# Optimization experiments

Measured on AMD Instinct MI355X. Metric: run time of the kernel, lower is better.

Reference implementation:

```python
import jax, jax.numpy as jnp
import numpy as np

GX, GY, GZ = 128, 128, 16   # voxel_range
N = 100000                  # occupied voxels
C = 64                      # channels (inc == outc)
K = 27                      # 3x3x3 kernel offsets
EPS = 1e-5
NEG_SLOPE = 0.01            # LeakyReLU default


def _kernel_map():
    """Build sparse-conv neighbor map: nbr[k, n] = row index of the input voxel at
    coord[n] + offset[k], or N (sentinel -> zero feature) if unoccupied/out of range."""
    rng = np.random.RandomState(0)
    flat = rng.choice(GX * GY * GZ, size=N, replace=False)
    x = flat // (GY * GZ)
    rem = flat % (GY * GZ)
    y = rem // GZ
    z = rem % GZ
    lut = np.full(GX * GY * GZ, N, dtype=np.int32)
    lut[flat] = np.arange(N, dtype=np.int32)
    offs = [(i, j, k) for i in (-1, 0, 1) for j in (-1, 0, 1) for k in (-1, 0, 1)]
    nbr = np.full((K, N), N, dtype=np.int32)
    for ki, (dx, dy, dz) in enumerate(offs):
        xs, ys, zs = x + dx, y + dy, z + dz
        valid = (xs >= 0) & (xs < GX) & (ys >= 0) & (ys < GY) & (zs >= 0) & (zs < GZ)
        fl = (np.clip(xs, 0, GX - 1) * (GY * GZ)
              + np.clip(ys, 0, GY - 1) * GZ
              + np.clip(zs, 0, GZ - 1))
        nbr[ki] = np.where(valid, lut[fl], N)
    return jnp.asarray(nbr)


def setup_inputs() -> dict:
    key = jax.random.key(0)
    k0, k1, k2 = jax.random.split(key, 3)
    w_scale = 1.0 / np.sqrt(C * K)  # Minkowski-style fan-in init
    return {
        "feats": jax.random.normal(k0, (N, C), jnp.float32),
        "W1": jax.random.normal(k1, (K, C, C), jnp.float32) * w_scale,
        "g1": jnp.ones((C,), jnp.float32),
        "b1": jnp.zeros((C,), jnp.float32),
        "W2": jax.random.normal(k2, (K, C, C), jnp.float32) * w_scale,
        "g2": jnp.ones((C,), jnp.float32),
        "b2": jnp.zeros((C,), jnp.float32),
        "nbr_idx": _kernel_map(),
    }


def _sparse_conv(f, W, nbr):
    # gather-GEMM-scatter: fp has a zero sentinel row at index N
    fp = jnp.concatenate([f, jnp.zeros((1, f.shape[1]), f.dtype)], axis=0)
    g = fp[nbr]                                # [K, N, Cin] gathered neighbors
    return jnp.einsum('knc,kco->no', g, W)     # [N, Cout]


def _bn(x, gamma, beta):
    # training-mode BatchNorm over all active voxels, per channel
    m = jnp.mean(x, axis=0)
    v = jnp.var(x, axis=0)
    return (x - m) * jax.lax.rsqrt(v + EPS) * gamma + beta


def _lrelu(x):
    return jnp.where(x >= 0, x, NEG_SLOPE * x)


def reference(feats, W1, g1, b1, W2, g2, b2, nbr_idx):
    skip = feats  # downsample is identity (inc == outc, stride == 1)
    y = _lrelu(_bn(_sparse_conv(feats, W1, nbr_idx), g1, b1))
    y = _lrelu(_bn(_sparse_conv(y, W2, nbr_idx), g2, b2))
    return _lrelu(skip + y)
```

## Files before the change

kernel.cpp:

```cpp
#include <hip/hip_runtime.h>
#include <hip/hip_bf16.h>


#define N_VOX 100000
#define NCH 64
#define NK 27
#define ROWS 128
#define NBLK ((N_VOX + ROWS - 1) / ROWS)

typedef __hip_bfloat16 bf16;
typedef __attribute__((ext_vector_type(8))) short bf16x8;
typedef __attribute__((ext_vector_type(4))) float f32x4;

__device__ __forceinline__ float b2f(short s) {
  unsigned u = ((unsigned)(unsigned short)s) << 16;
  return __builtin_bit_cast(float, u);
}
__device__ __forceinline__ short f2b(float f) {
  __hip_bfloat16 h = __float2bfloat16(f);
  return __builtin_bit_cast(short, h);
}

__device__ __forceinline__ void gload16(const void* g, void* l) {
  __builtin_amdgcn_global_load_lds(
      (const __attribute__((address_space(1))) void*)g,
      (__attribute__((address_space(3))) void*)l, 16, 0, 0);
}

__global__ void cast_feats(const float* __restrict__ feats, bf16* __restrict__ fbf) {
  const size_t i = ((size_t)blockIdx.x * 256 + threadIdx.x) * 8;
  if (i >= (size_t)(N_VOX + 1) * NCH) return;
  bf16x8 o;
  if (i < (size_t)N_VOX * NCH) {
    const f32x4 v0 = *reinterpret_cast<const f32x4*>(feats + i);
    const f32x4 v1 = *reinterpret_cast<const f32x4*>(feats + i + 4);
#pragma unroll
    for (int e = 0; e < 8; ++e) o[e] = f2b(e < 4 ? v0[e] : v1[e - 4]);
  } else {
#pragma unroll
    for (int e = 0; e < 8; ++e) o[e] = 0;
  }
  *reinterpret_cast<bf16x8*>((short*)fbf + i) = o;
}

__global__ void pack_w(const float* __restrict__ W1, const float* __restrict__ W2,
                       bf16* __restrict__ wp1, bf16* __restrict__ wp2) {
  const int t = blockIdx.x * 256 + threadIdx.x;
  const int half = NK * 4 * 2 * 64;
  if (t >= 2 * half) return;
  const float* W = (t < half) ? W1 : W2;
  short* wp = (short*)((t < half) ? wp1 : wp2);
  const int q = (t < half) ? t : t - half;
  const int l  = q & 63;
  const int kb = (q >> 6) & 1;
  const int j  = (q >> 7) & 3;
  const int k  = q >> 9;
  const int oo = j * 16 + (l & 15);
  const int c0 = kb * 32 + (l >> 4) * 8;
  bf16x8 v;
#pragma unroll
  for (int e = 0; e < 8; ++e)
    v[e] = f2b(W[((size_t)k * 64 + c0 + e) * 64 + oo]);
  *reinterpret_cast<bf16x8*>(&wp[(size_t)q * 8]) = v;
}

__global__ __launch_bounds__(256, 2)
void conv_mfma(const bf16* __restrict__ feat, const bf16* __restrict__ wp,
               const int* __restrict__ nbr, bf16* __restrict__ y,
               float* __restrict__ part) {
  __shared__ short GA[2][ROWS * NCH];
  __shared__ short GB[2][8 * 512];
  __shared__ int nbrL[NK * ROWS];
  __shared__ float redS[4][NCH];
  __shared__ float redQ[4][NCH];

  const int tid = threadIdx.x;
  const int lane = tid & 63;
  const int wv = tid >> 6;

  const int nwg = NBLK;
  const int xcd = blockIdx.x & 7;
  const int pos = blockIdx.x >> 3;
  const int q8 = nwg >> 3, r8 = nwg & 7;
  const int bid = (xcd < r8 ? xcd * (q8 + 1) : r8 * (q8 + 1) + (xcd - r8) * q8) + pos;
  const int n0 = bid * ROWS;

  for (int t = tid; t < NK * ROWS; t += 256) {
    const int k = t >> 7;
    const int rr = t & (ROWS - 1);
    nbrL[t] = (n0 + rr < N_VOX) ? nbr[(size_t)k * N_VOX + n0 + rr] : N_VOX;
  }
  __syncthreads();

  f32x4 acc[2][4];
#pragma unroll
  for (int h = 0; h < 2; ++h)
#pragma unroll
    for (int j = 0; j < 4; ++j)
      acc[h][j] = (f32x4){0.f, 0.f, 0.f, 0.f};

  auto stage = [&](int buf, int k) {
#pragma unroll
    for (int i = 0; i < 4; ++i) {
      const int s = i * 256 + wv * 64 + lane;
      const int row = s >> 3;
      const int p = (s & 7) ^ (row & 7);
      const int idx = nbrL[k * ROWS + row];
      const bf16* src = feat + (size_t)idx * NCH + p * 8;
      gload16((const void*)src, (void*)&GA[buf][(i * 256 + wv * 64) * 8]);
    }
#pragma unroll
    for (int t = 0; t < 2; ++t) {
      const int f = wv * 2 + t;
      const short* src = (const short*)wp + ((size_t)k * 8 + f) * 512 + lane * 8;
      gload16((const void*)src, (void*)&GB[buf][f * 512]);
    }
  };

  stage(0, 0);
  stage(1, 1);

  for (int k = 0; k < NK; ++k) {
    if (k < NK - 1) asm volatile("s_waitcnt vmcnt(6)" ::: "memory");
    else            asm volatile("s_waitcnt vmcnt(0)" ::: "memory");
    __builtin_amdgcn_sched_barrier(0);
    __builtin_amdgcn_s_barrier();

    const int cur = k & 1;

    bf16x8 Bf[4][2];
#pragma unroll
    for (int j = 0; j < 4; ++j)
#pragma unroll
      for (int kb = 0; kb < 2; ++kb)
        Bf[j][kb] = *reinterpret_cast<const bf16x8*>(
            &GB[cur][(j * 2 + kb) * 512 + lane * 8]);

    bf16x8 Af[2][2];
#pragma unroll
    for (int h = 0; h < 2; ++h)
#pragma unroll
      for (int kb = 0; kb < 2; ++kb) {
        const int rr = wv * 32 + h * 16 + (lane & 15);
        const int p = (kb * 4 + (lane >> 4)) ^ (rr & 7);
        Af[h][kb] = *reinterpret_cast<const bf16x8*>(&GA[cur][rr * NCH + p * 8]);
      }

#pragma unroll
    for (int h = 0; h < 2; ++h)
#pragma unroll
      for (int j = 0; j < 4; ++j)
#pragma unroll
        for (int kb = 0; kb < 2; ++kb)
          acc[h][j] = __builtin_amdgcn_mfma_f32_16x16x32_bf16(
              Af[h][kb], Bf[j][kb], acc[h][j], 0, 0, 0);

    __builtin_amdgcn_s_barrier();
    __builtin_amdgcn_sched_barrier(0);
    if (k + 2 < NK) stage(cur, k + 2);
  }

#pragma unroll
  for (int h = 0; h < 2; ++h)
#pragma unroll
    for (int j = 0; j < 4; ++j) {
      const int col = j * 16 + (lane & 15);
#pragma unroll
      for (int r = 0; r < 4; ++r) {
        const int row = n0 + wv * 32 + h * 16 + (lane >> 4) * 4 + r;
        if (row < N_VOX) ((short*)y)[(size_t)row * NCH + col] = f2b(acc[h][j][r]);
      }
    }

#pragma unroll
  for (int j = 0; j < 4; ++j) {
    float s1 = 0.f, s2 = 0.f;
#pragma unroll
    for (int h = 0; h < 2; ++h)
#pragma unroll
      for (int r = 0; r < 4; ++r) {
        const float v = acc[h][j][r];
        s1 += v;
        s2 += v * v;
      }
    s1 += __shfl_xor(s1, 16); s2 += __shfl_xor(s2, 16);
    s1 += __shfl_xor(s1, 32); s2 += __shfl_xor(s2, 32);
    if (lane < 16) {
      redS[wv][j * 16 + lane] = s1;
      redQ[wv][j * 16 + lane] = s2;
    }
  }
  __syncthreads();
  if (tid < NCH) {
    const float s1 = redS[0][tid] + redS[1][tid] + redS[2][tid] + redS[3][tid];
    const float s2 = redQ[0][tid] + redQ[1][tid] + redQ[2][tid] + redQ[3][tid];
    part[(size_t)blockIdx.x * 128 + tid] = s1;
    part[(size_t)blockIdx.x * 128 + 64 + tid] = s2;
  }
}

__global__ void finalize(const float* __restrict__ part, int nblk,
                         const float* __restrict__ g, const float* __restrict__ b,
                         float* __restrict__ ab) {
  __shared__ float r1[256], r2[256];
  const int c = blockIdx.x;
  const int t = threadIdx.x;
  float s1 = 0.f, s2 = 0.f;
  for (int bb = t; bb < nblk; bb += 256) {
    s1 += part[(size_t)bb * 128 + c];
    s2 += part[(size_t)bb * 128 + 64 + c];
  }
  r1[t] = s1; r2[t] = s2;
  __syncthreads();
  for (int off = 128; off > 0; off >>= 1) {
    if (t < off) { r1[t] += r1[t + off]; r2[t] += r2[t + off]; }
    __syncthreads();
  }
  if (t == 0) {
    const float m = r1[0] / (float)N_VOX;
    const float v = r2[0] / (float)N_VOX - m * m;
    const float a = g[c] * rsqrtf(v + 1e-5f);
    const float sh = b[c] - m * a;
    ab[c] = a;
    ab[64 + c] = sh;
  }
}

__global__ void bn_act(const bf16* __restrict__ y, const float* __restrict__ ab,
                       bf16* __restrict__ z) {
  const size_t i = ((size_t)blockIdx.x * 256 + threadIdx.x) * 8;
  if (i >= (size_t)(N_VOX + 1) * NCH) return;
  const int col = (int)(i & 63);
  bf16x8 o;
  if (i < (size_t)N_VOX * NCH) {
    const bf16x8 v = *reinterpret_cast<const bf16x8*>((const short*)y + i);
#pragma unroll
    for (int e = 0; e < 8; ++e) {
      float x = b2f(v[e]) * ab[col + e] + ab[64 + col + e];
      x = x < 0.f ? 0.01f * x : x;
      o[e] = f2b(x);
    }
  } else {
#pragma unroll
    for (int e = 0; e < 8; ++e) o[e] = 0;
  }
  *reinterpret_cast<bf16x8*>((short*)z + i) = o;
}

__global__ void bn_act_res(const bf16* __restrict__ y, const float* __restrict__ ab,
                           const float* __restrict__ feats, float* __restrict__ out) {
  const size_t i = ((size_t)blockIdx.x * 256 + threadIdx.x) * 8;
  const int col = (int)(i & 63);
  const bf16x8 v = *reinterpret_cast<const bf16x8*>((const short*)y + i);
  const f32x4 s0 = *reinterpret_cast<const f32x4*>(feats + i);
  const f32x4 s1 = *reinterpret_cast<const f32x4*>(feats + i + 4);
  f32x4 o0, o1;
#pragma unroll
  for (int e = 0; e < 8; ++e) {
    float x = b2f(v[e]) * ab[col + e] + ab[64 + col + e];
    x = x < 0.f ? 0.01f * x : x;
    float r = (e < 4 ? s0[e] : s1[e - 4]) + x;
    r = r < 0.f ? 0.01f * r : r;
    if (e < 4) o0[e] = r; else o1[e - 4] = r;
  }
  *reinterpret_cast<f32x4*>(out + i) = o0;
  *reinterpret_cast<f32x4*>(out + i + 4) = o1;
}

extern "C" void kernel_launch(void* const* d_in, const int* in_sizes, int n_in,
                              void* d_out, int out_size, void* d_ws, size_t ws_size,
                              hipStream_t stream) {
  const float* feats = (const float*)d_in[0];
  const float* W1 = (const float*)d_in[1];
  const float* g1 = (const float*)d_in[2];
  const float* b1 = (const float*)d_in[3];
  const float* W2 = (const float*)d_in[4];
  const float* g2 = (const float*)d_in[5];
  const float* b2 = (const float*)d_in[6];
  const int* nbr = (const int*)d_in[7];
  float* out = (float*)d_out;

  char* p = (char*)d_ws;
  bf16* fbf = (bf16*)p; p += (size_t)(N_VOX + 1) * NCH * 2;
  bf16* ybf = (bf16*)p; p += (size_t)N_VOX * NCH * 2;
  bf16* z = (bf16*)p;   p += (size_t)(N_VOX + 1) * NCH * 2;
  bf16* wp1 = (bf16*)p; p += 442368;
  bf16* wp2 = (bf16*)p; p += 442368;
  float* part = (float*)p; p += (size_t)NBLK * 128 * 4;
  float* ab1 = (float*)p; p += 512;
  float* ab2 = (float*)p; p += 512;

  const int cast_blocks = (int)(((size_t)(N_VOX + 1) * NCH / 8 + 255) / 256);

  cast_feats<<<cast_blocks, 256, 0, stream>>>(feats, fbf);
  pack_w<<<108, 256, 0, stream>>>(W1, W2, wp1, wp2);

  conv_mfma<<<NBLK, 256, 0, stream>>>(fbf, wp1, nbr, ybf, part);
  finalize<<<64, 256, 0, stream>>>(part, NBLK, g1, b1, ab1);
  bn_act<<<cast_blocks, 256, 0, stream>>>(ybf, ab1, z);

  conv_mfma<<<NBLK, 256, 0, stream>>>(z, wp2, nbr, ybf, part);
  finalize<<<64, 256, 0, stream>>>(part, NBLK, g2, b2, ab2);
  bn_act_res<<<(N_VOX * NCH / 8) / 256, 256, 0, stream>>>(ybf, ab2, feats, out);
}
```

Before: 144.8 us.

## Load weight fragments directly into registers and drop LDS weight staging

Removes the LDS double buffer for pre-packed weights and instead loads each offset's B fragments straight from global memory into two alternating register sets (even/odd offsets), prefetched two steps ahead alongside the gathered feature tiles. The wait count is adjusted to account for the extra in-flight vector loads. This cuts LDS traffic and shared memory per block, allowing the launch bound to request three blocks per CU. The trade-off is 16 extra bf16x8 registers per thread, which may cause spills under the tighter register budget, plus redundant per-wave global weight reads.

```diff
diff --git a/kernel.cpp b/kernel.cpp
--- a/kernel.cpp
+++ b/kernel.cpp
@@ -64,12 +64,11 @@
   *reinterpret_cast<bf16x8*>(&wp[(size_t)q * 8]) = v;
 }
 
-__global__ __launch_bounds__(256, 2)
+__global__ __launch_bounds__(256, 3)
 void conv_mfma(const bf16* __restrict__ feat, const bf16* __restrict__ wp,
                const int* __restrict__ nbr, bf16* __restrict__ y,
                float* __restrict__ part) {
   __shared__ short GA[2][ROWS * NCH];
-  __shared__ short GB[2][8 * 512];
   __shared__ int nbrL[NK * ROWS];
   __shared__ float redS[4][NCH];
   __shared__ float redQ[4][NCH];
@@ -109,33 +108,22 @@
       const bf16* src = feat + (size_t)idx * NCH + p * 8;
       gload16((const void*)src, (void*)&GA[buf][(i * 256 + wv * 64) * 8]);
     }
-#pragma unroll
-    for (int t = 0; t < 2; ++t) {
-      const int f = wv * 2 + t;
-      const short* src = (const short*)wp + ((size_t)k * 8 + f) * 512 + lane * 8;
-      gload16((const void*)src, (void*)&GB[buf][f * 512]);
-    }
   };
 
-  stage(0, 0);
-  stage(1, 1);
-
-  for (int k = 0; k < NK; ++k) {
-    if (k < NK - 1) asm volatile("s_waitcnt vmcnt(6)" ::: "memory");
+  auto loadB = [&](bf16x8 (&Bf)[8], int k) {
+#pragma unroll
+    for (int f = 0; f < 8; ++f)
+      Bf[f] = *reinterpret_cast<const bf16x8*>(
+          (const short*)wp + ((size_t)k * 8 + f) * 512 + lane * 8);
+  };
+
+  auto tile_step = [&](int k, bf16x8 (&Bf)[8]) {
+    if (k < NK - 1) asm volatile("s_waitcnt vmcnt(12)" ::: "memory");
     else            asm volatile("s_waitcnt vmcnt(0)" ::: "memory");
     __builtin_amdgcn_sched_barrier(0);
     __builtin_amdgcn_s_barrier();
 
     const int cur = k & 1;
-
-    bf16x8 Bf[4][2];
-#pragma unroll
-    for (int j = 0; j < 4; ++j)
-#pragma unroll
-      for (int kb = 0; kb < 2; ++kb)
-        Bf[j][kb] = *reinterpret_cast<const bf16x8*>(
-            &GB[cur][(j * 2 + kb) * 512 + lane * 8]);
-
     bf16x8 Af[2][2];
 #pragma unroll
     for (int h = 0; h < 2; ++h)
@@ -153,11 +141,25 @@
 #pragma unroll
         for (int kb = 0; kb < 2; ++kb)
           acc[h][j] = __builtin_amdgcn_mfma_f32_16x16x32_bf16(
-              Af[h][kb], Bf[j][kb], acc[h][j], 0, 0, 0);
+              Af[h][kb], Bf[j * 2 + kb], acc[h][j], 0, 0, 0);
 
     __builtin_amdgcn_s_barrier();
     __builtin_amdgcn_sched_barrier(0);
-    if (k + 2 < NK) stage(cur, k + 2);
+    if (k + 2 < NK) {
+      stage(cur, k + 2);
+      loadB(Bf, k + 2);
+    }
+  };
+
+  bf16x8 BfE[8], BfO[8];
+  loadB(BfE, 0);
+  stage(0, 0);
+  stage(1, 1);
+  loadB(BfO, 1);
+
+  for (int t = 0; t < 14; ++t) {
+    tile_step(2 * t, BfE);
+    if (2 * t + 1 < NK) tile_step(2 * t + 1, BfO);
   }
 
 #pragma unroll
```

Result: slower. 155.7 us (+7.5%).
